# Performance work log

Hardware: AMD Instinct MI355X
Metric: run time of the kernel (lower is better)

Reference implementation:

```python
import jax, jax.numpy as jnp
import numpy as np

H8, W8 = 64, 64
H4, W4 = 128, 128
C_LAT, C_HI = 256, 128
N_Q = 1024
ORIG_H, ORIG_W = 512, 512
NUM_ITERS = 4
TEMP = 20.0
DIM = 4 + C_HI + C_LAT        # 388 mixer output dim
IN_DIM = DIM + 3 * 49         # 535 mixer input dim
HID = 512


def _unit(v):
    return v / jnp.sqrt(jnp.maximum(jnp.sum(v * v, axis=-1, keepdims=True), 1e-12))


def setup_inputs() -> dict:
    key = jax.random.key(0)
    ks = jax.random.split(key, 20)
    fg = _unit(jax.random.normal(ks[0], (1, H8, W8, C_LAT), jnp.float32))
    hg = _unit(jax.random.normal(ks[1], (1, H4, W4, C_HI), jnp.float32))
    qf = _unit(jax.random.normal(ks[2], (1, N_Q, C_LAT), jnp.float32))
    hq = _unit(jax.random.normal(ks[3], (1, N_Q, C_HI), jnp.float32))
    p = lambda k, s, sc=0.05: sc * jax.random.normal(k, s, jnp.float32)
    return dict(
        feature_grid=fg, hires_feats_grid=hg, query_feats=qf, hires_query_feats=hq,
        hid1_w=p(ks[4], (16, 1, 3, 3)), hid1_b=jnp.zeros((16,), jnp.float32),
        hid2_w=p(ks[5], (1, 16, 3, 3)), hid2_b=jnp.zeros((1,), jnp.float32),
        hid3_w=p(ks[6], (32, 16, 3, 3)), hid3_b=jnp.zeros((32,), jnp.float32),
        hid4_w=p(ks[7], (32, 16)), hid4_b=jnp.zeros((16,), jnp.float32),
        occ_w=p(ks[8], (16, 2)), occ_b=jnp.zeros((2,), jnp.float32),
        mix_in_w=p(ks[9], (IN_DIM, HID), 0.02), mix_in_b=jnp.zeros((HID,), jnp.float32),
        mix_out_w=p(ks[10], (HID, DIM), 0.02), mix_out_b=jnp.zeros((DIM,), jnp.float32),
    )


def _conv2d(x, w, b, stride, pad):
    y = jax.lax.conv_general_dilated(x, w, (stride, stride), pad,
                                     dimension_numbers=('NCHW', 'OIHW', 'NCHW'))
    return y + b[None, :, None, None]


def _bilinear_sample(grid, coords):
    # grid [H,W,C]; coords [..., 2] as (y, x); edge-clamped bilinear gather.
    H, W = grid.shape[0], grid.shape[1]
    y, x = coords[..., 0], coords[..., 1]
    y0f, x0f = jnp.floor(y), jnp.floor(x)
    wy, wx = (y - y0f)[..., None], (x - x0f)[..., None]
    y0 = jnp.clip(y0f.astype(jnp.int32), 0, H - 1)
    y1 = jnp.clip(y0f.astype(jnp.int32) + 1, 0, H - 1)
    x0 = jnp.clip(x0f.astype(jnp.int32), 0, W - 1)
    x1 = jnp.clip(x0f.astype(jnp.int32) + 1, 0, W - 1)
    g00, g01 = grid[y0, x0], grid[y0, x1]
    g10, g11 = grid[y1, x0], grid[y1, x1]
    return (g00 * (1 - wy) * (1 - wx) + g01 * (1 - wy) * wx
            + g10 * wy * (1 - wx) + g11 * wy * wx)


def _forward(fg, hg, qf, hq, hid1_w, hid1_b, hid2_w, hid2_b, hid3_w, hid3_b,
             hid4_w, hid4_b, occ_w, occ_b, mix_in_w, mix_in_b, mix_out_w, mix_out_b):
    # --- tracks_from_cost_volume ---
    cv = jnp.einsum('bnc,bhwc->bnhw', qf, fg)                 # [1,N,64,64]
    b, n, h, w = cv.shape
    x = cv.reshape(b * n, 1, h, w)
    occ_map = jax.nn.relu(_conv2d(x, hid1_w, hid1_b, 1, 'SAME'))   # [bn,16,h,w]
    pmap = _conv2d(occ_map, hid2_w, hid2_b, 1, 'SAME').reshape(b * n, h * w)
    heat = jax.nn.softmax(pmap * TEMP, axis=-1).reshape(b * n, h, w)
    ey = jnp.einsum('bhw,h->b', heat, jnp.arange(h, dtype=jnp.float32))
    ex = jnp.einsum('bhw,w->b', heat, jnp.arange(w, dtype=jnp.float32))
    points = jnp.stack([ex * (ORIG_W / w), ey * (ORIG_H / h)], -1).reshape(b, n, 2)
    op = jnp.pad(occ_map, ((0, 0), (0, 0), (0, 2), (0, 2)))
    o3 = jax.nn.relu(_conv2d(op, hid3_w, hid3_b, 2, 'VALID'))
    o3 = o3.mean((-1, -2))                                     # [bn,32]
    o3 = jax.nn.relu(o3 @ hid4_w + hid4_b)
    o3 = (o3 @ occ_w + occ_b).reshape(b, n, 2)
    occ, expd = o3[..., 0], o3[..., 1]

    # --- iterative pips refinement ---
    cy, cx = jnp.meshgrid(jnp.arange(-3, 4), jnp.arange(-3, 4), indexing='ij')
    ctx = jnp.stack([cy, cx], -1).reshape(-1, 2).astype(jnp.float32)   # [49,2] (dy,dx)
    fg_avg = fg.reshape(1, H8 // 2, 2, W8 // 2, 2, C_LAT).mean((2, 4))
    pyramid = [hg, fg, fg_avg]
    feats = jnp.concatenate([hq, qf], -1)                      # [1,N,384]
    pos = points
    for it in range(NUM_ITERS):
        if it == 0:
            queries = [hq[0], qf[0], qf[0]]
        else:
            queries = [feats[0, :, :C_HI], feats[0, :, C_HI:], feats[0, :, C_HI:]]
        corrs = []
        for grid, q in zip(pyramid, queries):
            gh, gw = grid.shape[1], grid.shape[2]
            scale = jnp.array([gw / ORIG_W, gh / ORIG_H], jnp.float32)
            c = (pos[0] * scale)[:, ::-1]                      # (x,y)->(y,x), [N,2]
            coords2 = c[:, None, :] + ctx[None]                # [N,49,2]
            nb = _bilinear_sample(grid[0], coords2)            # [N,49,C]
            corrs.append(jnp.einsum('nsc,nc->ns', nb, q))
        corrs = jnp.concatenate(corrs, -1)[None]               # [1,N,147]
        mlp_in = jnp.concatenate([jnp.zeros_like(pos), occ[..., None],
                                  expd[..., None], feats, corrs], -1)
        res = jax.nn.gelu(mlp_in @ mix_in_w + mix_in_b) @ mix_out_w + mix_out_b
        pos = pos + res[..., :2]
        occ = occ + res[..., 2]
        expd = expd + res[..., 3]
        feats = feats + res[..., 4:]
    return jnp.concatenate([pos, occ[..., None], expd[..., None]], -1)  # [1,N,4]


def reference(feature_grid, hires_feats_grid, query_feats, hires_query_feats,
              hid1_w, hid1_b, hid2_w, hid2_b, hid3_w, hid3_b, hid4_w, hid4_b,
              occ_w, occ_b, mix_in_w, mix_in_b, mix_out_w, mix_out_b):
    return _forward(feature_grid, hires_feats_grid, query_feats, hires_query_feats,
                    hid1_w, hid1_b, hid2_w, hid2_b, hid3_w, hid3_b, hid4_w, hid4_b,
                    occ_w, occ_b, mix_in_w, mix_in_b, mix_out_w, mix_out_b)
```

## Files before the change

### kernel.cpp

```cpp
#include <hip/hip_runtime.h>
#include <hip/hip_bf16.h>
#include <math.h>


#define NQ 1024
#define TEMPF 20.0f
#define DIMV 388
#define INDIM 535
#define KPAD 544
#define HID 512

#define WS_CVB     0
#define WS_WIT     2097152
#define WS_WOT     2236416
#define WS_FG16    2351104
#define WS_HG16    2875392
#define WS_AV16    3923968
#define WS_FGAVG   4194304
#define WS_POS     (WS_FGAVG + 262144)
#define WS_OCC     (WS_POS + NQ*2)
#define WS_EXPD    (WS_OCC + NQ)
#define WS_FEATS   (WS_EXPD + NQ)
#define WS_MLPIN   (WS_FEATS + NQ*384)
#define WS_HIDDEN  (WS_MLPIN + NQ*KPAD)
#define WS_W3B     (WS_HIDDEN + NQ*HID)
#define WS_PART    (WS_MLPIN + 278528)
#define WS_SUM3    WS_HIDDEN

#define OP 72
#define CVP 68

typedef __attribute__((ext_vector_type(8))) short bf16x8;
typedef __attribute__((ext_vector_type(4))) float f32x4;

union BU8 { uint4 u; __hip_bfloat16 h[8]; };

__global__ __launch_bounds__(256) void k_prep_cv(
    const float* __restrict__ fg, const float* __restrict__ hg,
    const float* __restrict__ qf, const float* __restrict__ hq,
    const float* __restrict__ w3, const float* __restrict__ wi,
    const float* __restrict__ wo, float* __restrict__ ws) {
  __shared__ __hip_bfloat16 A_s[32 * 32];
  __shared__ __hip_bfloat16 B_s[64 * 32];
  const int bx = blockIdx.x;
  const int t = threadIdx.x;

  if (bx >= 2048) {
    int i = (bx - 2048) * 256 + t;
    if (i < 262144) {
      int c = i & 255, ox = (i >> 8) & 31, oy = i >> 13;
      const float* b = fg + (((oy * 2) * 64 + ox * 2) << 8) + c;
      float av = 0.25f * (b[0] + b[256] + b[16384] + b[16384 + 256]);
      ((__hip_bfloat16*)(ws + WS_AV16))[i] = __float2bfloat16(av);
    } else if (i < 655360) {
      int j = i - 262144;
      int n = j / 384, c = j - n * 384;
      float v = (c < 128) ? hq[n * 128 + c] : qf[n * 256 + c - 128];
      ws[WS_FEATS + j] = v;
      __hip_bfloat16* mi = (__hip_bfloat16*)(ws + WS_MLPIN);
      mi[n * KPAD + 4 + c] = __float2bfloat16(v);
      if (c == 0) {
        mi[n * KPAD + 0] = __float2bfloat16(0.f);
        mi[n * KPAD + 1] = __float2bfloat16(0.f);
      }
    } else if (i < 660480) {
      int j = i - 655360;
      int e = j & 7, qd = (j >> 3) & 3, nl = (j >> 5) & 15;
      int nt = (j >> 9) & 1, kt = j >> 10;
      int k = kt * 32 + qd * 8 + e;
      int ic = k & 15, tap = k >> 4;
      int oc = nt * 16 + nl;
      float v = (tap < 9) ? w3[(oc * 16 + ic) * 9 + tap] : 0.f;
      ((__hip_bfloat16*)(ws + WS_W3B))[j] = __float2bfloat16(v);
    } else if (i < 1184768) {
      ws[WS_SUM3 + (i - 660480)] = 0.f;
    } else if (i < 1463296) {
      int j = i - 1184768;
      int n = j / KPAD, k = j - n * KPAD;
      float v = (k < INDIM) ? wi[k * HID + n] : 0.f;
      ((__hip_bfloat16*)(ws + WS_WIT))[j] = __float2bfloat16(v);
    } else if (i < 1692672) {
      int j = i - 1463296;
      int n = j >> 9, k = j & 511;
      float v = (n < DIMV) ? wo[k * DIMV + n] : 0.f;
      ((__hip_bfloat16*)(ws + WS_WOT))[j] = __float2bfloat16(v);
    } else if (i < 1954816) {
      int j = (i - 1692672) * 4;
      float4 v = *(const float4*)&fg[j];
      union { __hip_bfloat16 h[4]; uint2 u; } pk;
      pk.h[0] = __float2bfloat16(v.x); pk.h[1] = __float2bfloat16(v.y);
      pk.h[2] = __float2bfloat16(v.z); pk.h[3] = __float2bfloat16(v.w);
      *(uint2*)(((__hip_bfloat16*)(ws + WS_FG16)) + j) = pk.u;
    } else {
      int j = (i - 1954816) * 4;
      float4 v = *(const float4*)&hg[j];
      union { __hip_bfloat16 h[4]; uint2 u; } pk;
      pk.h[0] = __float2bfloat16(v.x); pk.h[1] = __float2bfloat16(v.y);
      pk.h[2] = __float2bfloat16(v.z); pk.h[3] = __float2bfloat16(v.w);
      *(uint2*)(((__hip_bfloat16*)(ws + WS_HG16)) + j) = pk.u;
    }
    return;
  }

  const int wv = t >> 6, lane = t & 63;
  const int wm = wv & 1, wn = wv >> 1;
  const int quad = lane >> 4, nl = lane & 15;
  const int p0 = (bx & 63) * 64, m0 = (bx >> 6) * 32;
  f32x4 acc0 = {0.f, 0.f, 0.f, 0.f};
  f32x4 acc1 = {0.f, 0.f, 0.f, 0.f};

  for (int k0 = 0; k0 < 256; k0 += 32) {
    {
      int r = t >> 3, c = t & 7;
      float4 v = *(const float4*)&qf[(m0 + r) * 256 + k0 + c * 4];
      union { __hip_bfloat16 h[4]; uint2 u; } pk;
      pk.h[0] = __float2bfloat16(v.x); pk.h[1] = __float2bfloat16(v.y);
      pk.h[2] = __float2bfloat16(v.z); pk.h[3] = __float2bfloat16(v.w);
      *(uint2*)&A_s[r * 32 + c * 4] = pk.u;
    }
    {
      int r = t >> 2, c = t & 3;
      const float* src = &fg[(p0 + r) * 256 + k0 + c * 8];
      float4 v0 = *(const float4*)src;
      float4 v1 = *(const float4*)(src + 4);
      union { __hip_bfloat16 h[8]; uint4 u; } pk;
      pk.h[0] = __float2bfloat16(v0.x); pk.h[1] = __float2bfloat16(v0.y);
      pk.h[2] = __float2bfloat16(v0.z); pk.h[3] = __float2bfloat16(v0.w);
      pk.h[4] = __float2bfloat16(v1.x); pk.h[5] = __float2bfloat16(v1.y);
      pk.h[6] = __float2bfloat16(v1.z); pk.h[7] = __float2bfloat16(v1.w);
      *(uint4*)&B_s[r * 32 + c * 8] = pk.u;
    }
    __syncthreads();
    bf16x8 a = *(const bf16x8*)&A_s[(16 * wm + nl) * 32 + quad * 8];
    bf16x8 b0 = *(const bf16x8*)&B_s[(32 * wn + nl) * 32 + quad * 8];
    bf16x8 b1 = *(const bf16x8*)&B_s[(32 * wn + 16 + nl) * 32 + quad * 8];
    acc0 = __builtin_amdgcn_mfma_f32_16x16x32_bf16(a, b0, acc0, 0, 0, 0);
    acc1 = __builtin_amdgcn_mfma_f32_16x16x32_bf16(a, b1, acc1, 0, 0, 0);
    __syncthreads();
  }
  __hip_bfloat16* cvb = (__hip_bfloat16*)ws;
#pragma unroll
  for (int nt = 0; nt < 2; nt++) {
    int n = p0 + 32 * wn + nt * 16 + nl;
#pragma unroll
    for (int r = 0; r < 4; r++) {
      int m = m0 + 16 * wm + quad * 4 + r;
      cvb[m * 4096 + n] = __float2bfloat16(nt ? acc1[r] : acc0[r]);
    }
  }
}

__global__ __launch_bounds__(256, 5) void k_head_stripe(
    const float* __restrict__ h1w, const float* __restrict__ h1b,
    const float* __restrict__ h2w, const float* __restrict__ h2b,
    const float* __restrict__ h3b, float* __restrict__ ws) {
  __shared__ float cvs[8 * CVP];
  __shared__ float occ[6 * 16 * OP];

  const int bx = blockIdx.x;
  const int q = bx >> 4, st = bx & 15;
  const int y0 = st * 4;
  const int t = threadIdx.x;
  const int wv = t >> 6, lane = t & 63;
  const int role = (wv + bx) & 3;
  const __hip_bfloat16* cvb = (const __hip_bfloat16*)ws + q * 4096;

  if (t < 192) {
    int rc = t >> 1, side = t & 1;
    *(float4*)&occ[rc * OP + side * 68] = make_float4(0.f, 0.f, 0.f, 0.f);
  }
  if (st == 0 || st == 15) {
    int r = (st == 0) ? 0 : 5;
    for (int i = t; i < 16 * 18; i += 256)
      *(float4*)&occ[(r * 16 + (i / 18)) * OP + (i % 18) * 4] =
          make_float4(0.f, 0.f, 0.f, 0.f);
  }
#pragma unroll
  for (int j = 0; j < 2; j++) {
    int i = t + 256 * j;
    int lr = i >> 6, x = i & 63;
    int g = y0 - 2 + lr;
    cvs[lr * CVP + x + 1] =
        (g >= 0 && g < 64) ? __bfloat162float(cvb[g * 64 + x]) : 0.f;
  }
  if (t < 32) {
    int rr = t >> 2, c = t & 3;
    cvs[rr * CVP + ((c == 0) ? 0 : (64 + c))] = 0.f;
  }
  __syncthreads();

  {
    const int x = lane;
    const int chg = wv * 4;
    float w1r[4][9], b1r[4];
#pragma unroll
    for (int k = 0; k < 4; k++) {
      b1r[k] = h1b[chg + k];
#pragma unroll
      for (int j = 0; j < 9; j++) w1r[k][j] = h1w[(chg + k) * 9 + j];
    }
    float win[3][3];
#pragma unroll
    for (int j = 0; j < 3; j++) {
      const float* cp = &cvs[j * CVP + x];
      win[j][0] = cp[0]; win[j][1] = cp[1]; win[j][2] = cp[2];
    }
    for (int r = 0; r < 6; r++) {
      if (r > 0) {
#pragma unroll
        for (int c = 0; c < 3; c++) { win[0][c] = win[1][c]; win[1][c] = win[2][c]; }
        const float* cp = &cvs[(r + 2) * CVP + x];
        win[2][0] = cp[0]; win[2][1] = cp[1]; win[2][2] = cp[2];
      }
      int yo = y0 - 1 + r;
      if (yo >= 0 && yo <= 63) {
#pragma unroll
        for (int k = 0; k < 4; k++) {
          float a = b1r[k];
#pragma unroll
          for (int ky = 0; ky < 3; ky++)
            a += w1r[k][3 * ky] * win[ky][0] + w1r[k][3 * ky + 1] * win[ky][1] +
                 w1r[k][3 * ky + 2] * win[ky][2];
          occ[(r * 16 + chg + k) * OP + x + 4] = fmaxf(a, 0.f);
        }
      }
    }
  }
  __syncthreads();

  if (role == 1 || role == 2) {
    const __hip_bfloat16* W3B = (const __hip_bfloat16*)(ws + WS_W3B);
    const int oyl = role - 1;
    const int nl = lane & 15;
    const int qd = lane >> 4, qh = qd >> 1, ql = qd & 1;
    f32x4 acc00 = {0.f,0.f,0.f,0.f}, acc01 = {0.f,0.f,0.f,0.f};
    f32x4 acc10 = {0.f,0.f,0.f,0.f}, acc11 = {0.f,0.f,0.f,0.f};
#pragma unroll
    for (int kt = 0; kt < 5; kt++) {
      int tap = kt * 2 + qh;
      int tv = (tap < 9) ? tap : 0;
      int ky = (tv >= 6) ? 2 : ((tv >= 3) ? 1 : 0);
      int kx = tv - 3 * ky;
      const float* ap =
          &occ[((2 * oyl + 1 + ky) * 16 + ql * 8) * OP + 4 + kx + 2 * nl];
      union { bf16x8 v; __hip_bfloat16 h[8]; } a0u, a1u;
      if (tap < 9) {
#pragma unroll
        for (int j = 0; j < 8; j++) {
          a0u.h[j] = __float2bfloat16(ap[j * OP]);
          a1u.h[j] = __float2bfloat16(ap[j * OP + 32]);
        }
      } else {
#pragma unroll
        for (int j = 0; j < 8; j++) {
          a0u.h[j] = __float2bfloat16(0.f);
          a1u.h[j] = __float2bfloat16(0.f);
        }
      }
      bf16x8 b0 = *(const bf16x8*)&W3B[((kt * 2 + 0) * 16 + nl) * 32 + qd * 8];
      bf16x8 b1 = *(const bf16x8*)&W3B[((kt * 2 + 1) * 16 + nl) * 32 + qd * 8];
      acc00 = __builtin_amdgcn_mfma_f32_16x16x32_bf16(a0u.v, b0, acc00, 0, 0, 0);
      acc01 = __builtin_amdgcn_mfma_f32_16x16x32_bf16(a0u.v, b1, acc01, 0, 0, 0);
      acc10 = __builtin_amdgcn_mfma_f32_16x16x32_bf16(a1u.v, b0, acc10, 0, 0, 0);
      acc11 = __builtin_amdgcn_mfma_f32_16x16x32_bf16(a1u.v, b1, acc11, 0, 0, 0);
    }
    float bb0 = h3b[nl], bb1 = h3b[16 + nl];
    float s0 = 0.f, s1 = 0.f;
#pragma unroll
    for (int r = 0; r < 4; r++) {
      s0 += fmaxf(acc00[r] + bb0, 0.f) + fmaxf(acc10[r] + bb0, 0.f);
      s1 += fmaxf(acc01[r] + bb1, 0.f) + fmaxf(acc11[r] + bb1, 0.f);
    }
    s0 += __shfl_xor(s0, 16); s0 += __shfl_xor(s0, 32);
    s1 += __shfl_xor(s1, 16); s1 += __shfl_xor(s1, 32);
    if (lane < 16) {
      atomicAdd(&ws[WS_SUM3 + (q * 16 + st) * 32 + nl], s0);
      atomicAdd(&ws[WS_SUM3 + (q * 16 + st) * 32 + 16 + nl], s1);
    }
  } else {
    const int rl = ((role == 3) ? 2 : 0) + (lane >> 5);
    const int yg = y0 + rl;
    const int xa = lane & 31;
    const int xb = xa + 32;
    float pa = 0.f, pb = 0.f;
    for (int ch = 0; ch < 16; ch++) {
#pragma unroll
      for (int ky = 0; ky < 3; ky++) {
        const float* bp = &occ[((rl + ky) * 16 + ch) * OP];
        float wa = h2w[ch * 9 + 3 * ky], wb = h2w[ch * 9 + 3 * ky + 1],
              wc = h2w[ch * 9 + 3 * ky + 2];
        pa += wa * bp[xa + 3] + wb * bp[xa + 4] + wc * bp[xa + 5];
        pb += wa * bp[xb + 3] + wb * bp[xb + 4] + wc * bp[xb + 5];
      }
    }
    float bb = h2b[0];
    float v0 = (pa + bb) * TEMPF, v1 = (pb + bb) * TEMPF;
    float mg = fmaxf(v0, v1);
#pragma unroll
    for (int off = 1; off < 64; off <<= 1) mg = fmaxf(mg, __shfl_xor(mg, off));
    float e0 = __expf(v0 - mg), e1 = __expf(v1 - mg);
    float s = e0 + e1;
    float sx = e0 * (float)xa + e1 * (float)xb;
    float sy = s * (float)yg;
#pragma unroll
    for (int off = 1; off < 64; off <<= 1) {
      s += __shfl_xor(s, off);
      sx += __shfl_xor(sx, off);
      sy += __shfl_xor(sy, off);
    }
    if (lane == 0) {
      int slot = q * 32 + st * 2 + ((role == 3) ? 1 : 0);
      *(float4*)&ws[WS_PART + slot * 4] = make_float4(mg, s, sx, sy);
    }
  }
}

__global__ __launch_bounds__(256) void k_merge(
    const float* __restrict__ w4, const float* __restrict__ b4,
    const float* __restrict__ w5, const float* __restrict__ b5,
    float* __restrict__ ws) {
  __shared__ float sums_s[4][32];
  __shared__ float o4s[4][16];
  int t = threadIdx.x, wv = t >> 6, lane = t & 63;
  int q = blockIdx.x * 4 + wv;

  float M = -1e30f, S = 0.f, SX = 0.f, SY = 0.f;
  if (lane < 32) {
    float4 pv = *(const float4*)&ws[WS_PART + (q * 32 + lane) * 4];
    M = pv.x; S = pv.y; SX = pv.z; SY = pv.w;
  }
#pragma unroll
  for (int off = 1; off < 64; off <<= 1) {
    float Mo = __shfl_xor(M, off), So = __shfl_xor(S, off);
    float SXo = __shfl_xor(SX, off), SYo = __shfl_xor(SY, off);
    float Mn = fmaxf(M, Mo);
    float c1 = __expf(M - Mn), c2 = __expf(Mo - Mn);
    S = S * c1 + So * c2; SX = SX * c1 + SXo * c2; SY = SY * c1 + SYo * c2;
    M = Mn;
  }
  if (lane == 0) {
    ws[WS_POS + q * 2 + 0] = (SX / S) * 8.0f;
    ws[WS_POS + q * 2 + 1] = (SY / S) * 8.0f;
  }

  int ch = lane & 31, half = lane >> 5;
  float sm = 0.f;
#pragma unroll
  for (int s8 = 0; s8 < 8; s8++)
    sm += ws[WS_SUM3 + (q * 16 + half * 8 + s8) * 32 + ch];
  sm += __shfl_xor(sm, 32);
  if (lane < 32) sums_s[wv][lane] = sm * (1.f / 1024.f);
  __syncthreads();
  if (lane < 16) {
    float a = b4[lane];
#pragma unroll
    for (int i = 0; i < 32; i++) a += sums_s[wv][i] * w4[i * 16 + lane];
    o4s[wv][lane] = fmaxf(a, 0.f);
  }
  __syncthreads();
  if (lane < 2) {
    float r = b5[lane];
#pragma unroll
    for (int j = 0; j < 16; j++) r += o4s[wv][j] * w5[j * 2 + lane];
    __hip_bfloat16* mi = (__hip_bfloat16*)(ws + WS_MLPIN);
    if (lane == 0) { ws[WS_OCC + q] = r;  mi[q * KPAD + 2] = __float2bfloat16(r); }
    else           { ws[WS_EXPD + q] = r; mi[q * KPAD + 3] = __float2bfloat16(r); }
  }
}

__global__ __launch_bounds__(256) void k_corr(float* __restrict__ ws) {
  __shared__ float qs[384];
  __shared__ float dbuf[3][64];
  int t = threadIdx.x;
  int wv = t >> 6, lane = t & 63;
  int cl = lane & 15, sub = lane >> 4;
  int n = blockIdx.x;
  const float* feats = ws + WS_FEATS + n * 384;
  float posx = ws[WS_POS + n * 2 + 0];
  float posy = ws[WS_POS + n * 2 + 1];
  __hip_bfloat16* mi = (__hip_bfloat16*)(ws + WS_MLPIN) + n * KPAD;

  for (int col = t; col < 384; col += 256) qs[col] = feats[col];
  __syncthreads();

  float qh[8], qq[16];
#pragma unroll
  for (int j = 0; j < 8; j++) qh[j] = qs[cl * 8 + j];
#pragma unroll
  for (int j = 0; j < 16; j++) qq[j] = qs[128 + cl * 16 + j];

  const __hip_bfloat16* G0 = (const __hip_bfloat16*)(ws + WS_HG16);
  const __hip_bfloat16* G1 = (const __hip_bfloat16*)(ws + WS_FG16);
  const __hip_bfloat16* G2 = (const __hip_bfloat16*)(ws + WS_AV16);

#pragma unroll
  for (int L = 0; L < 3; L++) {
    const __hip_bfloat16* grid;
    int Hg, Wg;
    float scl;
    if (L == 0)      { grid = G0; Hg = 128; Wg = 128; scl = 0.25f; }
    else if (L == 1) { grid = G1; Hg = 64;  Wg = 64;  scl = 0.125f; }
    else             { grid = G2; Hg = 32;  Wg = 32;  scl = 0.0625f; }
    float cy = posy * scl, cx = posx * scl;
    int iy = (int)floorf(cy), ix = (int)floorf(cx);
#pragma unroll
    for (int g = 0; g < 4; g++) {
      int p = wv * 16 + g * 4 + sub;
      int a = p >> 3, b = p & 7;
      int row = iy + a - 3; row = row < 0 ? 0 : (row > Hg - 1 ? Hg - 1 : row);
      int col = ix + b - 3; col = col < 0 ? 0 : (col > Wg - 1 ? Wg - 1 : col);
      float acc = 0.f;
      if (L == 0) {
        BU8 g0; g0.u = *(const uint4*)(grid + (row * Wg + col) * 128 + cl * 8);
#pragma unroll
        for (int j = 0; j < 8; j++) acc += __bfloat162float(g0.h[j]) * qh[j];
      } else {
        const __hip_bfloat16* gp = grid + (row * Wg + col) * 256 + cl * 16;
        BU8 g0, g1;
        g0.u = *(const uint4*)gp;
        g1.u = *(const uint4*)(gp + 8);
#pragma unroll
        for (int j = 0; j < 8; j++) {
          acc += __bfloat162float(g0.h[j]) * qq[j];
          acc += __bfloat162float(g1.h[j]) * qq[8 + j];
        }
      }
      acc += __shfl_xor(acc, 1);
      acc += __shfl_xor(acc, 2);
      acc += __shfl_xor(acc, 4);
      acc += __shfl_xor(acc, 8);
      if (cl == 0) dbuf[L][p] = acc;
    }
  }
  __syncthreads();

  if (t < 147) {
    int L = t / 49, s = t - L * 49;
    int sa = s / 7, sb = s - sa * 7;
    float scl = (L == 0) ? 0.25f : ((L == 1) ? 0.125f : 0.0625f);
    float cy = posy * scl, cx = posx * scl;
    float wy = cy - floorf(cy), wx = cx - floorf(cx);
    int i00 = sa * 8 + sb;
    float d00 = dbuf[L][i00], d01 = dbuf[L][i00 + 1];
    float d10 = dbuf[L][i00 + 8], d11 = dbuf[L][i00 + 9];
    float corr = (1.f - wy) * (1.f - wx) * d00 + (1.f - wy) * wx * d01 +
                 wy * (1.f - wx) * d10 + wy * wx * d11;
    mi[388 + t] = __float2bfloat16(corr);
  }
}

__device__ __forceinline__ float gelu_tanh(float x) {
  float z = 0.7978845608028654f * (x + 0.044715f * x * x * x);
  z = fminf(fmaxf(z, -15.f), 15.f);
  float e = __expf(2.f * z);
  float th = (e - 1.f) / (e + 1.f);
  return 0.5f * x * (1.f + th);
}

__global__ __launch_bounds__(256) void k_mix1(
    const float* __restrict__ bias, float* __restrict__ ws) {
  const int t = threadIdx.x;
  const int wv = t >> 6, lane = t & 63;
  const int nt = blockIdx.x * 4 + wv;
  const int mt = blockIdx.y;
  const int m0 = mt * 16, n0 = nt * 16;
  const int nl = lane & 15, quad = lane >> 4;
  const unsigned short* Abf = (const unsigned short*)(ws + WS_MLPIN);
  const unsigned short* WIT = (const unsigned short*)(ws + WS_WIT);
  const unsigned short* ap = &Abf[(m0 + nl) * KPAD + quad * 8];
  const unsigned short* bp = &WIT[(n0 + nl) * KPAD + quad * 8];
  f32x4 acc = {0.f, 0.f, 0.f, 0.f};
#pragma unroll
  for (int ks = 0; ks < 17; ks++) {
    bf16x8 a = *(const bf16x8*)(ap + ks * 32);
    bf16x8 b = *(const bf16x8*)(bp + ks * 32);
    acc = __builtin_amdgcn_mfma_f32_16x16x32_bf16(a, b, acc, 0, 0, 0);
  }
  __hip_bfloat16* Hd = (__hip_bfloat16*)(ws + WS_HIDDEN);
  int nn = n0 + nl;
  float bv = bias[nn];
#pragma unroll
  for (int r = 0; r < 4; r++) {
    int m = m0 + quad * 4 + r;
    Hd[m * HID + nn] = __float2bfloat16(gelu_tanh(acc[r] + bv));
  }
}

__global__ __launch_bounds__(256) void k_mix2(
    const float* __restrict__ bias, float* __restrict__ ws,
    float* __restrict__ out) {
  const int t = threadIdx.x;
  const int wv = t >> 6, lane = t & 63;
  const int nt = blockIdx.x * 4 + wv;
  const int mt = blockIdx.y;
  const int m0 = mt * 16, n0 = nt * 16;
  const int nl = lane & 15, quad = lane >> 4;
  const unsigned short* Abf = (const unsigned short*)(ws + WS_HIDDEN);
  const unsigned short* WOT = (const unsigned short*)(ws + WS_WOT);
  const unsigned short* ap = &Abf[(m0 + nl) * HID + quad * 8];
  const unsigned short* bp = &WOT[(n0 + nl) * HID + quad * 8];
  f32x4 acc = {0.f, 0.f, 0.f, 0.f};
#pragma unroll
  for (int ks = 0; ks < 16; ks++) {
    bf16x8 a = *(const bf16x8*)(ap + ks * 32);
    bf16x8 b = *(const bf16x8*)(bp + ks * 32);
    acc = __builtin_amdgcn_mfma_f32_16x16x32_bf16(a, b, acc, 0, 0, 0);
  }

  int col = n0 + nl;
  if (col < DIMV) {
    float bv = bias[col];
    __hip_bfloat16* mib = (__hip_bfloat16*)(ws + WS_MLPIN);
#pragma unroll
    for (int r = 0; r < 4; r++) {
      int m = m0 + quad * 4 + r;
      float rr = acc[r] + bv;
      if (col < 2) {
        float v = ws[WS_POS + m * 2 + col] + rr;
        ws[WS_POS + m * 2 + col] = v;
        out[m * 4 + col] = v;
      } else if (col == 2) {
        float v = ws[WS_OCC + m] + rr;
        ws[WS_OCC + m] = v;
        out[m * 4 + 2] = v;
        mib[m * KPAD + 2] = __float2bfloat16(v);
      } else if (col == 3) {
        float v = ws[WS_EXPD + m] + rr;
        ws[WS_EXPD + m] = v;
        out[m * 4 + 3] = v;
        mib[m * KPAD + 3] = __float2bfloat16(v);
      } else {
        float v = ws[WS_FEATS + m * 384 + (col - 4)] + rr;
        ws[WS_FEATS + m * 384 + (col - 4)] = v;
        mib[m * KPAD + col] = __float2bfloat16(v);
      }
    }
  }
}

extern "C" void kernel_launch(void* const* d_in, const int* in_sizes, int n_in,
                              void* d_out, int out_size, void* d_ws, size_t ws_size,
                              hipStream_t stream) {
  const float* fg = (const float*)d_in[0];
  const float* hg = (const float*)d_in[1];
  const float* qf = (const float*)d_in[2];
  const float* hq = (const float*)d_in[3];
  const float* w1 = (const float*)d_in[4];
  const float* b1 = (const float*)d_in[5];
  const float* w2 = (const float*)d_in[6];
  const float* b2 = (const float*)d_in[7];
  const float* w3 = (const float*)d_in[8];
  const float* b3 = (const float*)d_in[9];
  const float* w4 = (const float*)d_in[10];
  const float* b4 = (const float*)d_in[11];
  const float* w5 = (const float*)d_in[12];
  const float* b5 = (const float*)d_in[13];
  const float* wi = (const float*)d_in[14];
  const float* bi = (const float*)d_in[15];
  const float* wo = (const float*)d_in[16];
  const float* bo = (const float*)d_in[17];
  float* ws = (float*)d_ws;
  float* out = (float*)d_out;

  k_prep_cv<<<11732, 256, 0, stream>>>(fg, hg, qf, hq, w3, wi, wo, ws);
  k_head_stripe<<<16384, 256, 0, stream>>>(w1, b1, w2, b2, b3, ws);
  k_merge<<<256, 256, 0, stream>>>(w4, b4, w5, b5, ws);
  for (int it = 0; it < 4; it++) {
    k_corr<<<1024, 256, 0, stream>>>(ws);
    k_mix1<<<dim3(8, 64), 256, 0, stream>>>(bi, ws);
    k_mix2<<<dim3(7, 64), 256, 0, stream>>>(bo, ws, out);
  }
}
```

Measured before the change: 309.9 us.

## Store conv1 activations as swizzled bf16 and run conv2 on MFMA

The intermediate conv1 output in shared memory changes from padded fp32 to a channel-interleaved, XOR-swizzled bf16 layout, so MFMA A-fragments for conv3 load as single 16-byte vectors instead of eight scalar loads plus conversions. The 16→1 conv2 is recast as an MFMA GEMM using pre-packed bf16 weights built in the prep kernel, and the softmax reduction is reorganised around the MFMA output layout. This targets LDS traffic, shared memory footprint and scalar FMA work in the head kernel. In exchange it lowers conv2 precision to bf16, which can shift the temperature-scaled softmax, and wastes MFMA lanes since conv2 has one output channel.

```diff
diff --git a/kernel.cpp b/kernel.cpp
--- a/kernel.cpp
+++ b/kernel.cpp
@@ -24,22 +24,30 @@
 #define WS_MLPIN   (WS_FEATS + NQ*384)
 #define WS_HIDDEN  (WS_MLPIN + NQ*KPAD)
 #define WS_W3B     (WS_HIDDEN + NQ*HID)
+#define WS_W2B     (WS_W3B + 2560)
 #define WS_PART    (WS_MLPIN + 278528)
 #define WS_SUM3    WS_HIDDEN
 
-#define OP 72
 #define CVP 68
+#define ROWP 2368
 
 typedef __attribute__((ext_vector_type(8))) short bf16x8;
 typedef __attribute__((ext_vector_type(4))) float f32x4;
 
 union BU8 { uint4 u; __hip_bfloat16 h[8]; };
+
+__device__ __forceinline__ int occ_off(int r, int idx, int c) {
+  int o = idx * 32 + c * 2;
+  o ^= ((idx >> 2) & 3) << 4;
+  return r * ROWP + o;
+}
 
 __global__ __launch_bounds__(256) void k_prep_cv(
     const float* __restrict__ fg, const float* __restrict__ hg,
     const float* __restrict__ qf, const float* __restrict__ hq,
-    const float* __restrict__ w3, const float* __restrict__ wi,
-    const float* __restrict__ wo, float* __restrict__ ws) {
+    const float* __restrict__ w3, const float* __restrict__ w2,
+    const float* __restrict__ wi, const float* __restrict__ wo,
+    float* __restrict__ ws) {
   __shared__ __hip_bfloat16 A_s[32 * 32];
   __shared__ __hip_bfloat16 B_s[64 * 32];
   const int bx = blockIdx.x;
@@ -72,27 +80,34 @@
       int oc = nt * 16 + nl;
       float v = (tap < 9) ? w3[(oc * 16 + ic) * 9 + tap] : 0.f;
       ((__hip_bfloat16*)(ws + WS_W3B))[j] = __float2bfloat16(v);
-    } else if (i < 1184768) {
-      ws[WS_SUM3 + (i - 660480)] = 0.f;
-    } else if (i < 1463296) {
-      int j = i - 1184768;
+    } else if (i < 663040) {
+      int j = i - 660480;
+      int e = j & 7, qd = (j >> 3) & 3, kt = j >> 9;
+      int k = kt * 32 + qd * 8 + e;
+      int ch = k & 15, tap = k >> 4;
+      float v = (tap < 9) ? w2[ch * 9 + tap] : 0.f;
+      ((__hip_bfloat16*)(ws + WS_W2B))[j] = __float2bfloat16(v);
+    } else if (i < 1187328) {
+      ws[WS_SUM3 + (i - 663040)] = 0.f;
+    } else if (i < 1465856) {
+      int j = i - 1187328;
       int n = j / KPAD, k = j - n * KPAD;
       float v = (k < INDIM) ? wi[k * HID + n] : 0.f;
       ((__hip_bfloat16*)(ws + WS_WIT))[j] = __float2bfloat16(v);
-    } else if (i < 1692672) {
-      int j = i - 1463296;
+    } else if (i < 1695232) {
+      int j = i - 1465856;
       int n = j >> 9, k = j & 511;
       float v = (n < DIMV) ? wo[k * DIMV + n] : 0.f;
       ((__hip_bfloat16*)(ws + WS_WOT))[j] = __float2bfloat16(v);
-    } else if (i < 1954816) {
-      int j = (i - 1692672) * 4;
+    } else if (i < 1957376) {
+      int j = (i - 1695232) * 4;
       float4 v = *(const float4*)&fg[j];
       union { __hip_bfloat16 h[4]; uint2 u; } pk;
       pk.h[0] = __float2bfloat16(v.x); pk.h[1] = __float2bfloat16(v.y);
       pk.h[2] = __float2bfloat16(v.z); pk.h[3] = __float2bfloat16(v.w);
       *(uint2*)(((__hip_bfloat16*)(ws + WS_FG16)) + j) = pk.u;
     } else {
-      int j = (i - 1954816) * 4;
+      int j = (i - 1957376) * 4;
       float4 v = *(const float4*)&hg[j];
       union { __hip_bfloat16 h[4]; uint2 u; } pk;
       pk.h[0] = __float2bfloat16(v.x); pk.h[1] = __float2bfloat16(v.y);
@@ -152,10 +167,11 @@
 
 __global__ __launch_bounds__(256, 5) void k_head_stripe(
     const float* __restrict__ h1w, const float* __restrict__ h1b,
-    const float* __restrict__ h2w, const float* __restrict__ h2b,
-    const float* __restrict__ h3b, float* __restrict__ ws) {
+    const float* __restrict__ h2b, const float* __restrict__ h3b,
+    float* __restrict__ ws) {
   __shared__ float cvs[8 * CVP];
-  __shared__ float occ[6 * 16 * OP];
+  __shared__ float4 occ_t4[6 * ROWP / 16];
+  char* occ_t = (char*)occ_t4;
 
   const int bx = blockIdx.x;
   const int q = bx >> 4, st = bx & 15;
@@ -166,14 +182,14 @@
   const __hip_bfloat16* cvb = (const __hip_bfloat16*)ws + q * 4096;
 
   if (t < 192) {
-    int rc = t >> 1, side = t & 1;
-    *(float4*)&occ[rc * OP + side * 68] = make_float4(0.f, 0.f, 0.f, 0.f);
+    int r = t >> 5, j = t & 31;
+    int off = r * ROWP + ((j < 16) ? j * 8 : 2176 + (j - 16) * 8);
+    *(uint2*)(occ_t + off) = make_uint2(0u, 0u);
   }
   if (st == 0 || st == 15) {
     int r = (st == 0) ? 0 : 5;
-    for (int i = t; i < 16 * 18; i += 256)
-      *(float4*)&occ[(r * 16 + (i / 18)) * OP + (i % 18) * 4] =
-          make_float4(0.f, 0.f, 0.f, 0.f);
+    for (int i = t; i < 288; i += 256)
+      *(uint2*)(occ_t + r * ROWP + i * 8) = make_uint2(0u, 0u);
   }
 #pragma unroll
   for (int j = 0; j < 2; j++) {
@@ -214,6 +230,7 @@
       }
       int yo = y0 - 1 + r;
       if (yo >= 0 && yo <= 63) {
+        union { __hip_bfloat16 h[4]; uint2 u; } pk;
 #pragma unroll
         for (int k = 0; k < 4; k++) {
           float a = b1r[k];
@@ -221,48 +238,43 @@
           for (int ky = 0; ky < 3; ky++)
             a += w1r[k][3 * ky] * win[ky][0] + w1r[k][3 * ky + 1] * win[ky][1] +
                  w1r[k][3 * ky + 2] * win[ky][2];
-          occ[(r * 16 + chg + k) * OP + x + 4] = fmaxf(a, 0.f);
+          pk.h[k] = __float2bfloat16(fmaxf(a, 0.f));
         }
+        *(uint2*)(occ_t + occ_off(r, x + 4, chg)) = pk.u;
       }
     }
   }
   __syncthreads();
+
+  const int nl = lane & 15;
+  const int qd = lane >> 4, qh = qd >> 1, ql = qd & 1;
 
   if (role == 1 || role == 2) {
     const __hip_bfloat16* W3B = (const __hip_bfloat16*)(ws + WS_W3B);
     const int oyl = role - 1;
-    const int nl = lane & 15;
-    const int qd = lane >> 4, qh = qd >> 1, ql = qd & 1;
     f32x4 acc00 = {0.f,0.f,0.f,0.f}, acc01 = {0.f,0.f,0.f,0.f};
     f32x4 acc10 = {0.f,0.f,0.f,0.f}, acc11 = {0.f,0.f,0.f,0.f};
 #pragma unroll
     for (int kt = 0; kt < 5; kt++) {
       int tap = kt * 2 + qh;
-      int tv = (tap < 9) ? tap : 0;
-      int ky = (tv >= 6) ? 2 : ((tv >= 3) ? 1 : 0);
-      int kx = tv - 3 * ky;
-      const float* ap =
-          &occ[((2 * oyl + 1 + ky) * 16 + ql * 8) * OP + 4 + kx + 2 * nl];
-      union { bf16x8 v; __hip_bfloat16 h[8]; } a0u, a1u;
+      bf16x8 a0, a1;
       if (tap < 9) {
-#pragma unroll
-        for (int j = 0; j < 8; j++) {
-          a0u.h[j] = __float2bfloat16(ap[j * OP]);
-          a1u.h[j] = __float2bfloat16(ap[j * OP + 32]);
-        }
+        int ky = (tap >= 6) ? 2 : ((tap >= 3) ? 1 : 0);
+        int kx = tap - 3 * ky;
+        int R = 2 * oyl + 1 + ky;
+        int idx0 = 4 + kx + 2 * nl;
+        a0 = *(const bf16x8*)(occ_t + occ_off(R, idx0, ql * 8));
+        a1 = *(const bf16x8*)(occ_t + occ_off(R, idx0 + 32, ql * 8));
       } else {
-#pragma unroll
-        for (int j = 0; j < 8; j++) {
-          a0u.h[j] = __float2bfloat16(0.f);
-          a1u.h[j] = __float2bfloat16(0.f);
-        }
+        a0 = (bf16x8){0, 0, 0, 0, 0, 0, 0, 0};
+        a1 = a0;
       }
       bf16x8 b0 = *(const bf16x8*)&W3B[((kt * 2 + 0) * 16 + nl) * 32 + qd * 8];
       bf16x8 b1 = *(const bf16x8*)&W3B[((kt * 2 + 1) * 16 + nl) * 32 + qd * 8];
-      acc00 = __builtin_amdgcn_mfma_f32_16x16x32_bf16(a0u.v, b0, acc00, 0, 0, 0);
-      acc01 = __builtin_amdgcn_mfma_f32_16x16x32_bf16(a0u.v, b1, acc01, 0, 0, 0);
-      acc10 = __builtin_amdgcn_mfma_f32_16x16x32_bf16(a1u.v, b0, acc10, 0, 0, 0);
-      acc11 = __builtin_amdgcn_mfma_f32_16x16x32_bf16(a1u.v, b1, acc11, 0, 0, 0);
+      acc00 = __builtin_amdgcn_mfma_f32_16x16x32_bf16(a0, b0, acc00, 0, 0, 0);
+      acc01 = __builtin_amdgcn_mfma_f32_16x16x32_bf16(a0, b1, acc01, 0, 0, 0);
+      acc10 = __builtin_amdgcn_mfma_f32_16x16x32_bf16(a1, b0, acc10, 0, 0, 0);
+      acc11 = __builtin_amdgcn_mfma_f32_16x16x32_bf16(a1, b1, acc11, 0, 0, 0);
     }
     float bb0 = h3b[nl], bb1 = h3b[16 + nl];
     float s0 = 0.f, s1 = 0.f;
@@ -278,36 +290,72 @@
       atomicAdd(&ws[WS_SUM3 + (q * 16 + st) * 32 + 16 + nl], s1);
     }
   } else {
-    const int rl = ((role == 3) ? 2 : 0) + (lane >> 5);
-    const int yg = y0 + rl;
-    const int xa = lane & 31;
-    const int xb = xa + 32;
-    float pa = 0.f, pb = 0.f;
-    for (int ch = 0; ch < 16; ch++) {
-#pragma unroll
-      for (int ky = 0; ky < 3; ky++) {
-        const float* bp = &occ[((rl + ky) * 16 + ch) * OP];
-        float wa = h2w[ch * 9 + 3 * ky], wb = h2w[ch * 9 + 3 * ky + 1],
-              wc = h2w[ch * 9 + 3 * ky + 2];
-        pa += wa * bp[xa + 3] + wb * bp[xa + 4] + wc * bp[xa + 5];
-        pb += wa * bp[xb + 3] + wb * bp[xb + 4] + wc * bp[xb + 5];
-      }
-    }
-    float bb = h2b[0];
-    float v0 = (pa + bb) * TEMPF, v1 = (pb + bb) * TEMPF;
-    float mg = fmaxf(v0, v1);
-#pragma unroll
-    for (int off = 1; off < 64; off <<= 1) mg = fmaxf(mg, __shfl_xor(mg, off));
-    float e0 = __expf(v0 - mg), e1 = __expf(v1 - mg);
-    float s = e0 + e1;
-    float sx = e0 * (float)xa + e1 * (float)xb;
-    float sy = s * (float)yg;
-#pragma unroll
-    for (int off = 1; off < 64; off <<= 1) {
-      s += __shfl_xor(s, off);
-      sx += __shfl_xor(sx, off);
-      sy += __shfl_xor(sy, off);
-    }
+    const int rl0 = (role == 3) ? 2 : 0;
+    const __hip_bfloat16* W2B = (const __hip_bfloat16*)(ws + WS_W2B);
+    bf16x8 wb0 = *(const bf16x8*)&W2B[(0 * 16 + nl) * 32 + qd * 8];
+    bf16x8 wb1 = *(const bf16x8*)&W2B[(1 * 16 + nl) * 32 + qd * 8];
+    bf16x8 wb2 = *(const bf16x8*)&W2B[(2 * 16 + nl) * 32 + qd * 8];
+    bf16x8 wb3 = *(const bf16x8*)&W2B[(3 * 16 + nl) * 32 + qd * 8];
+    bf16x8 wb4 = *(const bf16x8*)&W2B[(4 * 16 + nl) * 32 + qd * 8];
+    f32x4 pa0 = {0.f,0.f,0.f,0.f}, pa1 = {0.f,0.f,0.f,0.f};
+    f32x4 pa2 = {0.f,0.f,0.f,0.f}, pa3 = {0.f,0.f,0.f,0.f};
+    f32x4 pa4 = {0.f,0.f,0.f,0.f}, pa5 = {0.f,0.f,0.f,0.f};
+    f32x4 pa6 = {0.f,0.f,0.f,0.f}, pa7 = {0.f,0.f,0.f,0.f};
+
+#define H2STEP(ACC, ROW, XT, KT, WB)                                         \
+    {                                                                        \
+      int tap = (KT) * 2 + qh;                                               \
+      bf16x8 a;                                                              \
+      if (tap < 9) {                                                         \
+        int ky = (tap >= 6) ? 2 : ((tap >= 3) ? 1 : 0);                      \
+        int kx = tap - 3 * ky;                                               \
+        a = *(const bf16x8*)(occ_t +                                         \
+            occ_off((ROW) + ky, (XT) + nl + 3 + kx, ql * 8));                \
+      } else { a = (bf16x8){0, 0, 0, 0, 0, 0, 0, 0}; }                       \
+      ACC = __builtin_amdgcn_mfma_f32_16x16x32_bf16(a, WB, ACC, 0, 0, 0);    \
+    }
+#define H2TILE(ACC, ROW, XT)                                                 \
+    H2STEP(ACC, ROW, XT, 0, wb0) H2STEP(ACC, ROW, XT, 1, wb1)                \
+    H2STEP(ACC, ROW, XT, 2, wb2) H2STEP(ACC, ROW, XT, 3, wb3)                \
+    H2STEP(ACC, ROW, XT, 4, wb4)
+
+    H2TILE(pa0, rl0, 0)      H2TILE(pa1, rl0, 16)
+    H2TILE(pa2, rl0, 32)     H2TILE(pa3, rl0, 48)
+    H2TILE(pa4, rl0 + 1, 0)  H2TILE(pa5, rl0 + 1, 16)
+    H2TILE(pa6, rl0 + 1, 32) H2TILE(pa7, rl0 + 1, 48)
+#undef H2TILE
+#undef H2STEP
+
+    const float bb = h2b[0];
+    float mg = -1e30f;
+#pragma unroll
+    for (int r = 0; r < 4; r++) {
+      mg = fmaxf(mg, fmaxf(fmaxf(pa0[r], pa1[r]), fmaxf(pa2[r], pa3[r])));
+      mg = fmaxf(mg, fmaxf(fmaxf(pa4[r], pa5[r]), fmaxf(pa6[r], pa7[r])));
+    }
+    mg = (mg + bb) * TEMPF;
+    mg = fmaxf(mg, __shfl_xor(mg, 16));
+    mg = fmaxf(mg, __shfl_xor(mg, 32));
+    float sa = 0.f, sb = 0.f, sx = 0.f;
+    const float fq = (float)(qd * 4);
+#pragma unroll
+    for (int r = 0; r < 4; r++) {
+      float xr = fq + (float)r;
+      float e;
+      e = __expf((pa0[r] + bb) * TEMPF - mg); sa += e; sx += e * (xr + 0.f);
+      e = __expf((pa1[r] + bb) * TEMPF - mg); sa += e; sx += e * (xr + 16.f);
+      e = __expf((pa2[r] + bb) * TEMPF - mg); sa += e; sx += e * (xr + 32.f);
+      e = __expf((pa3[r] + bb) * TEMPF - mg); sa += e; sx += e * (xr + 48.f);
+      e = __expf((pa4[r] + bb) * TEMPF - mg); sb += e; sx += e * (xr + 0.f);
+      e = __expf((pa5[r] + bb) * TEMPF - mg); sb += e; sx += e * (xr + 16.f);
+      e = __expf((pa6[r] + bb) * TEMPF - mg); sb += e; sx += e * (xr + 32.f);
+      e = __expf((pa7[r] + bb) * TEMPF - mg); sb += e; sx += e * (xr + 48.f);
+    }
+    float ya = (float)(y0 + rl0);
+    float s = sa + sb;
+    float sy = ya * sa + (ya + 1.f) * sb;
+    s += __shfl_xor(s, 16); sx += __shfl_xor(sx, 16); sy += __shfl_xor(sy, 16);
+    s += __shfl_xor(s, 32); sx += __shfl_xor(sx, 32); sy += __shfl_xor(sy, 32);
     if (lane == 0) {
       int slot = q * 32 + st * 2 + ((role == 3) ? 1 : 0);
       *(float4*)&ws[WS_PART + slot * 4] = make_float4(mg, s, sx, sy);
@@ -562,8 +610,8 @@
   float* ws = (float*)d_ws;
   float* out = (float*)d_out;
 
-  k_prep_cv<<<11732, 256, 0, stream>>>(fg, hg, qf, hq, w3, wi, wo, ws);
-  k_head_stripe<<<16384, 256, 0, stream>>>(w1, b1, w2, b2, b3, ws);
+  k_prep_cv<<<11742, 256, 0, stream>>>(fg, hg, qf, hq, w3, w2, wi, wo, ws);
+  k_head_stripe<<<16384, 256, 0, stream>>>(w1, b1, b2, b3, ws);
   k_merge<<<256, 256, 0, stream>>>(w4, b4, w5, b5, ws);
   for (int it = 0; it < 4; it++) {
     k_corr<<<1024, 256, 0, stream>>>(ws);
```

New measurement: 298.2 us, median of 2. 1.04x faster.
